# Optimization experiments

Measured on AMD Instinct MI355X. Metric: run time of the kernel, lower is better.

The kernel has to match this reference:

```python
import jax, jax.numpy as jnp
import numpy as np


def setup_inputs() -> dict:
    key = jax.random.key(0)
    k1, k2, k3 = jax.random.split(key, 3)
    B, C, H, W = 64, 512, 28, 28
    K = 32
    std = 1.0 / (K * C) ** 0.5
    x = jax.random.normal(k1, (B, C, H, W), dtype=jnp.float32)
    codewords = jax.random.uniform(k2, (K, C), dtype=jnp.float32, minval=-std, maxval=std)
    scale = jax.random.uniform(k3, (K,), dtype=jnp.float32, minval=-1.0, maxval=0.0)
    return {"x": x, "codewords": codewords, "scale": scale}


def reference(x, codewords, scale):
    # x: (B, C, H, W) -> descriptors (B, N, C)
    B, C, H, W = x.shape
    K = codewords.shape[0]
    xd = x.reshape(B, C, H * W).transpose(0, 2, 1)  # (B, N, C)

    # scaled L2: scale_k * ||x_n - c_k||^2, expanded without (B,N,K,C) intermediate
    x_sq = jnp.sum(xd * xd, axis=-1, keepdims=True)            # (B, N, 1)
    c_sq = jnp.sum(codewords * codewords, axis=-1)             # (K,)
    xc = jnp.einsum("bnc,kc->bnk", xd, codewords)              # (B, N, K)
    dist = scale * (x_sq - 2.0 * xc + c_sq)                    # (B, N, K)

    A = jax.nn.softmax(dist, axis=2)                           # (B, N, K)

    # encoded_k = sum_n A[b,n,k] * (x[b,n] - c[k])
    wx = jnp.einsum("bnk,bnc->bkc", A, xd)                     # (B, K, C)
    wsum = jnp.sum(A, axis=1)                                  # (B, K)
    encoded = wx - wsum[:, :, None] * codewords[None, :, :]    # (B, K, C)
    return encoded
```

## Files before the change

kernel.cpp:

```cpp
#include <hip/hip_runtime.h>

#define BB 64
#define CC 512
#define NPIX 784
#define KK 32
#define NSA 7
#define AS 800
#define CW_S 520
#define NSTEP 24

typedef __attribute__((ext_vector_type(8))) short short8;
typedef __attribute__((ext_vector_type(4))) float floatx4;
typedef __attribute__((ext_vector_type(16))) float floatx16;
typedef __attribute__((ext_vector_type(4))) unsigned short ushort4v;

#define WSUM_OFF (BB * KK * AS)

__device__ __forceinline__ unsigned short f2bf(float f) {
    union { float f; unsigned u; } v; v.f = f;
    return (unsigned short)((v.u + 0x7FFFu + ((v.u >> 16) & 1u)) >> 16);
}
__device__ __forceinline__ float bf2f(unsigned short h) {
    union { unsigned u; float f; } v; v.u = ((unsigned)h) << 16; return v.f;
}
__device__ __forceinline__ short8 pack8(const float4& a, const float4& b) {
    short8 r;
    r[0] = (short)f2bf(a.x); r[1] = (short)f2bf(a.y);
    r[2] = (short)f2bf(a.z); r[3] = (short)f2bf(a.w);
    r[4] = (short)f2bf(b.x); r[5] = (short)f2bf(b.y);
    r[6] = (short)f2bf(b.z); r[7] = (short)f2bf(b.w);
    return r;
}

__global__ __launch_bounds__(256, 4) void kA(const float* __restrict__ x,
                                             const float* __restrict__ cw,
                                             const float* __restrict__ scale,
                                             unsigned short* __restrict__ Ag)
{
    __shared__ __align__(16) unsigned short cs[KK * CW_S];
    __shared__ float csq_p[8][KK];
    __shared__ float csq_l[KK];
    __shared__ float wredA[4][KK];

    const int t    = threadIdx.x;
    const int lane = t & 63, w = t >> 6;
    const int pl   = lane & 31, h = lane >> 5;
    const int split = blockIdx.x, b = blockIdx.y;
    const int p0    = (split < 6) ? split * 128 : 656;
    const bool active = !(split == 6 && w < 3);

    if (split == 0 && t < 64) {
        const short8 z = {0, 0, 0, 0, 0, 0, 0, 0};
        const int k = t >> 1, off = (t & 1) * 8;
        *(short8*)&Ag[(size_t)b * KK * AS + (size_t)k * AS + NPIX + off] = z;
    }

#pragma unroll 4
    for (int j = 0; j < 16; ++j) {
        const int qidx = t + j * 256;
        const int row = qidx >> 7, qc = qidx & 127;
        const float4 v = *(const float4*)&cw[row * CC + qc * 4];
        ushort4v p; p.x = f2bf(v.x); p.y = f2bf(v.y); p.z = f2bf(v.z); p.w = f2bf(v.w);
        *(ushort4v*)&cs[row * CW_S + qc * 4] = p;
    }
    __syncthreads();
    {
        const int k = t & 31, part = t >> 5;
        float s = 0.f;
        for (int i = 0; i < 64; ++i) {
            const float v = bf2f(cs[k * CW_S + part * 64 + i]);
            s += v * v;
        }
        csq_p[part][k] = s;
    }
    __syncthreads();
    if (t < KK) {
        float s = 0.f;
#pragma unroll
        for (int p = 0; p < 8; ++p) s += csq_p[p][t];
        csq_l[t] = s;
    }
    __syncthreads();

    const float sk = scale[pl];
    const float qk = csq_l[pl];

    const int px = p0 + w * 32 + pl;
    const float* xb = x + (size_t)b * CC * NPIX + px;

    floatx16 acc = {0.f,0.f,0.f,0.f,0.f,0.f,0.f,0.f,0.f,0.f,0.f,0.f,0.f,0.f,0.f,0.f};
    float xsqp = 0.f;

    if (active) {
        float va[8], vb[8];
#pragma unroll
        for (int j = 0; j < 8; ++j) va[j] = xb[(size_t)(h * 8 + j) * NPIX];

#pragma unroll
        for (int kc = 0; kc < 32; kc += 2) {
            {
                const int cb = (kc + 1) * 16 + h * 8;
#pragma unroll
                for (int j = 0; j < 8; ++j) vb[j] = xb[(size_t)(cb + j) * NPIX];
            }
            {
                short8 a;
#pragma unroll
                for (int j = 0; j < 8; ++j) { xsqp += va[j] * va[j]; a[j] = (short)f2bf(va[j]); }
                const short8 bf = *(const short8*)&cs[pl * CW_S + kc * 16 + h * 8];
                acc = __builtin_amdgcn_mfma_f32_32x32x16_bf16(a, bf, acc, 0, 0, 0);
            }
            if (kc + 2 < 32) {
                const int cb = (kc + 2) * 16 + h * 8;
#pragma unroll
                for (int j = 0; j < 8; ++j) va[j] = xb[(size_t)(cb + j) * NPIX];
            }
            {
                short8 a;
#pragma unroll
                for (int j = 0; j < 8; ++j) { xsqp += vb[j] * vb[j]; a[j] = (short)f2bf(vb[j]); }
                const short8 bf = *(const short8*)&cs[pl * CW_S + (kc + 1) * 16 + h * 8];
                acc = __builtin_amdgcn_mfma_f32_32x32x16_bf16(a, bf, acc, 0, 0, 0);
            }
        }
    }

    const float xsqf = xsqp + __shfl_xor(xsqp, 32);

    unsigned short* Ab = Ag + (size_t)b * KK * AS + p0 + w * 32;
    float ts = 0.f;
    if (active) {
#pragma unroll
        for (int r = 0; r < 16; ++r) {
            const int pwr = (r & 3) + 8 * (r >> 2) + 4 * h;
            const float xq = __shfl(xsqf, pwr);
            const float d = sk * (xq + qk - 2.f * acc[r]);
            float mx = d;
            mx = fmaxf(mx, __shfl_xor(mx, 1));
            mx = fmaxf(mx, __shfl_xor(mx, 2));
            mx = fmaxf(mx, __shfl_xor(mx, 4));
            mx = fmaxf(mx, __shfl_xor(mx, 8));
            mx = fmaxf(mx, __shfl_xor(mx, 16));
            const float e = __expf(d - mx);
            float sm = e;
            sm += __shfl_xor(sm, 1);
            sm += __shfl_xor(sm, 2);
            sm += __shfl_xor(sm, 4);
            sm += __shfl_xor(sm, 8);
            sm += __shfl_xor(sm, 16);
            const float av = e * (1.f / sm);
            Ab[pl * AS + pwr] = f2bf(av);
            if (split < 6 || r >= 8) ts += av;
        }
    }
    ts += __shfl_xor(ts, 32);
    if (lane < 32) wredA[w][pl] = active ? ts : 0.f;
    __syncthreads();
    if (t < KK) {
        const float s = wredA[0][t] + wredA[1][t] + wredA[2][t] + wredA[3][t];
        float* wsf = (float*)(Ag + WSUM_OFF);
        wsf[(size_t)(split * BB + b) * KK + t] = s;
    }
}

__global__ __launch_bounds__(256) void kB(const float* __restrict__ x,
                                          const float* __restrict__ cw,
                                          const unsigned short* __restrict__ Ag,
                                          float* __restrict__ out)
{
    __shared__ float wsum_l[KK];

    const int t    = threadIdx.x;
    const int lane = t & 63, w = t >> 6;
    const int col  = lane & 15, quad = lane >> 4;
    const int cch  = blockIdx.x, b = blockIdx.y;

    const unsigned short* Ab = Ag + (size_t)b * KK * AS;

    if (t < KK) {
        const float* wsf = (const float*)(Ag + WSUM_OFF);
        float s = 0.f;
#pragma unroll
        for (int sp = 0; sp < NSA; ++sp) s += wsf[(size_t)(sp * BB + b) * KK + t];
        wsum_l[t] = s;
    }

    const int c = cch * 64 + w * 16 + col;
    const float* xp = x + ((size_t)b * CC + c) * NPIX;
    const unsigned short* a0p = Ab + (size_t)col * AS;
    const unsigned short* a1p = Ab + (size_t)(col + 16) * AS;
    const int qo = quad * 8;

    floatx4 acc0 = {0.f, 0.f, 0.f, 0.f};
    floatx4 acc1 = {0.f, 0.f, 0.f, 0.f};
#pragma unroll 6
    for (int s = 0; s < NSTEP; ++s) {
        const int off = s * 32 + qo;
        const short8 av0 = *(const short8*)&a0p[off];
        const short8 av1 = *(const short8*)&a1p[off];
        const float4 xv0 = *(const float4*)&xp[off];
        const float4 xv1 = *(const float4*)&xp[off + 4];
        const short8 bv = pack8(xv0, xv1);
        acc0 = __builtin_amdgcn_mfma_f32_16x16x32_bf16(av0, bv, acc0, 0, 0, 0);
        acc1 = __builtin_amdgcn_mfma_f32_16x16x32_bf16(av1, bv, acc1, 0, 0, 0);
    }
    {
        const int off = NSTEP * 32 + qo;
        const short8 av0 = *(const short8*)&a0p[off];
        const short8 av1 = *(const short8*)&a1p[off];
        float4 xv0 = make_float4(0.f, 0.f, 0.f, 0.f);
        float4 xv1 = make_float4(0.f, 0.f, 0.f, 0.f);
        if (quad < 2) {
            xv0 = *(const float4*)&xp[off];
            xv1 = *(const float4*)&xp[off + 4];
        }
        const short8 bv = pack8(xv0, xv1);
        acc0 = __builtin_amdgcn_mfma_f32_16x16x32_bf16(av0, bv, acc0, 0, 0, 0);
        acc1 = __builtin_amdgcn_mfma_f32_16x16x32_bf16(av1, bv, acc1, 0, 0, 0);
    }

    __syncthreads();

    float* ob = out + (size_t)b * KK * CC + c;
    const float* cp = cw + c;
#pragma unroll
    for (int r = 0; r < 4; ++r) {
        const int k0 = quad * 4 + r;
        ob[(size_t)k0 * CC]        = acc0[r] - wsum_l[k0]      * cp[(size_t)k0 * CC];
        ob[(size_t)(k0 + 16) * CC] = acc1[r] - wsum_l[k0 + 16] * cp[(size_t)(k0 + 16) * CC];
    }
}

extern "C" void kernel_launch(void* const* d_in, const int* in_sizes, int n_in,
                              void* d_out, int out_size, void* d_ws, size_t ws_size,
                              hipStream_t stream) {
    const float* x     = (const float*)d_in[0];
    const float* cw    = (const float*)d_in[1];
    const float* scale = (const float*)d_in[2];
    float* out = (float*)d_out;
    unsigned short* Ag = (unsigned short*)d_ws;

    kA<<<dim3(NSA, BB), dim3(256), 0, stream>>>(x, cw, scale, Ag);
    kB<<<dim3(8, BB), dim3(256), 0, stream>>>(x, cw, Ag, out);
}
```

Baseline: 181.3 us.

## Split channel reduction across wave pairs and double kA pixel splits

kA now gives each block 64 pixels instead of 128, so there are 13 pixel splits per batch instead of 7. Within a block, two waves per pixel tile each handle half of the 512 channels, and their MFMA partial sums and squared norms are combined through shared memory before one wave runs the softmax. This doubles the number of blocks and halves each wave's serial load-and-MFMA chain, aiming to hide memory latency better and keep more CUs busy. In exchange, each block repeats the codeword conversion, uses more LDS (occupancy bound lowered from 4 to 3), adds a barrier, and the overlapping last split writes some A values twice.

Result: slower. 185.4 us (+2.2%).

```diff
diff --git a/kernel.cpp b/kernel.cpp
--- a/kernel.cpp
+++ b/kernel.cpp
@@ -4,7 +4,7 @@
 #define CC 512
 #define NPIX 784
 #define KK 32
-#define NSA 7
+#define NSA 13
 #define AS 800
 #define CW_S 520
 #define NSTEP 24
@@ -32,22 +32,23 @@
     return r;
 }
 
-__global__ __launch_bounds__(256, 4) void kA(const float* __restrict__ x,
+__global__ __launch_bounds__(256, 3) void kA(const float* __restrict__ x,
                                              const float* __restrict__ cw,
                                              const float* __restrict__ scale,
                                              unsigned short* __restrict__ Ag)
 {
     __shared__ __align__(16) unsigned short cs[KK * CW_S];
+    __shared__ __align__(16) float accr[2][64][20];
     __shared__ float csq_p[8][KK];
     __shared__ float csq_l[KK];
-    __shared__ float wredA[4][KK];
+    __shared__ float wredA[2][KK];
 
     const int t    = threadIdx.x;
     const int lane = t & 63, w = t >> 6;
     const int pl   = lane & 31, h = lane >> 5;
+    const int tile = w & 1, ch = w >> 1;
     const int split = blockIdx.x, b = blockIdx.y;
-    const int p0    = (split < 6) ? split * 128 : 656;
-    const bool active = !(split == 6 && w < 3);
+    const int p0    = (split < 12) ? split * 64 : 720;
 
     if (split == 0 && t < 64) {
         const short8 z = {0, 0, 0, 0, 0, 0, 0, 0};
@@ -85,51 +86,63 @@
     const float sk = scale[pl];
     const float qk = csq_l[pl];
 
-    const int px = p0 + w * 32 + pl;
+    const int px = p0 + tile * 32 + pl;
     const float* xb = x + (size_t)b * CC * NPIX + px;
+    const int cbase = ch * 256;
 
     floatx16 acc = {0.f,0.f,0.f,0.f,0.f,0.f,0.f,0.f,0.f,0.f,0.f,0.f,0.f,0.f,0.f,0.f};
     float xsqp = 0.f;
-
-    if (active) {
-        float va[8], vb[8];
-#pragma unroll
-        for (int j = 0; j < 8; ++j) va[j] = xb[(size_t)(h * 8 + j) * NPIX];
-
-#pragma unroll
-        for (int kc = 0; kc < 32; kc += 2) {
-            {
-                const int cb = (kc + 1) * 16 + h * 8;
-#pragma unroll
-                for (int j = 0; j < 8; ++j) vb[j] = xb[(size_t)(cb + j) * NPIX];
-            }
-            {
-                short8 a;
-#pragma unroll
-                for (int j = 0; j < 8; ++j) { xsqp += va[j] * va[j]; a[j] = (short)f2bf(va[j]); }
-                const short8 bf = *(const short8*)&cs[pl * CW_S + kc * 16 + h * 8];
-                acc = __builtin_amdgcn_mfma_f32_32x32x16_bf16(a, bf, acc, 0, 0, 0);
-            }
-            if (kc + 2 < 32) {
-                const int cb = (kc + 2) * 16 + h * 8;
-#pragma unroll
-                for (int j = 0; j < 8; ++j) va[j] = xb[(size_t)(cb + j) * NPIX];
-            }
-            {
-                short8 a;
-#pragma unroll
-                for (int j = 0; j < 8; ++j) { xsqp += vb[j] * vb[j]; a[j] = (short)f2bf(vb[j]); }
-                const short8 bf = *(const short8*)&cs[pl * CW_S + (kc + 1) * 16 + h * 8];
-                acc = __builtin_amdgcn_mfma_f32_32x32x16_bf16(a, bf, acc, 0, 0, 0);
-            }
-        }
-    }
-
-    const float xsqf = xsqp + __shfl_xor(xsqp, 32);
-
-    unsigned short* Ab = Ag + (size_t)b * KK * AS + p0 + w * 32;
-    float ts = 0.f;
-    if (active) {
+    float va[8], vb[8];
+
+#pragma unroll
+    for (int j = 0; j < 8; ++j) va[j] = xb[(size_t)(cbase + h * 8 + j) * NPIX];
+
+#pragma unroll
+    for (int kc = 0; kc < 16; kc += 2) {
+        {
+            const int cb = cbase + (kc + 1) * 16 + h * 8;
+#pragma unroll
+            for (int j = 0; j < 8; ++j) vb[j] = xb[(size_t)(cb + j) * NPIX];
+        }
+        {
+            short8 a;
+#pragma unroll
+            for (int j = 0; j < 8; ++j) { xsqp += va[j] * va[j]; a[j] = (short)f2bf(va[j]); }
+            const short8 bf = *(const short8*)&cs[pl * CW_S + cbase + kc * 16 + h * 8];
+            acc = __builtin_amdgcn_mfma_f32_32x32x16_bf16(a, bf, acc, 0, 0, 0);
+        }
+        if (kc + 2 < 16) {
+            const int cb = cbase + (kc + 2) * 16 + h * 8;
+#pragma unroll
+            for (int j = 0; j < 8; ++j) va[j] = xb[(size_t)(cb + j) * NPIX];
+        }
+        {
+            short8 a;
+#pragma unroll
+            for (int j = 0; j < 8; ++j) { xsqp += vb[j] * vb[j]; a[j] = (short)f2bf(vb[j]); }
+            const short8 bf = *(const short8*)&cs[pl * CW_S + cbase + (kc + 1) * 16 + h * 8];
+            acc = __builtin_amdgcn_mfma_f32_32x32x16_bf16(a, bf, acc, 0, 0, 0);
+        }
+    }
+
+    const float xsqh = xsqp + __shfl_xor(xsqp, 32);
+
+    if (ch == 1) {
+#pragma unroll
+        for (int q = 0; q < 4; ++q)
+            *(floatx4*)&accr[tile][lane][q * 4] =
+                (floatx4){acc[q*4], acc[q*4+1], acc[q*4+2], acc[q*4+3]};
+        accr[tile][lane][16] = xsqh;
+    }
+    __syncthreads();
+
+    if (ch == 0) {
+#pragma unroll
+        for (int r = 0; r < 16; ++r) acc[r] += accr[tile][lane][r];
+        const float xsqf = xsqh + accr[tile][lane][16];
+
+        unsigned short* Ab = Ag + (size_t)b * KK * AS + p0 + tile * 32;
+        float ts = 0.f;
 #pragma unroll
         for (int r = 0; r < 16; ++r) {
             const int pwr = (r & 3) + 8 * (r >> 2) + 4 * h;
@@ -150,14 +163,15 @@
             sm += __shfl_xor(sm, 16);
             const float av = e * (1.f / sm);
             Ab[pl * AS + pwr] = f2bf(av);
-            if (split < 6 || r >= 8) ts += av;
-        }
-    }
-    ts += __shfl_xor(ts, 32);
-    if (lane < 32) wredA[w][pl] = active ? ts : 0.f;
+            if (split < 12) ts += av;
+            else if (tile == 1 && r >= 8) ts += av;
+        }
+        ts += __shfl_xor(ts, 32);
+        if (lane < 32) wredA[tile][pl] = ts;
+    }
     __syncthreads();
     if (t < KK) {
-        const float s = wredA[0][t] + wredA[1][t] + wredA[2][t] + wredA[3][t];
+        const float s = wredA[0][t] + wredA[1][t];
         float* wsf = (float*)(Ag + WSUM_OFF);
         wsf[(size_t)(split * BB + b) * KK + t] = s;
     }
```
